# Kernel tuning notes

Measured on AMD Instinct MI355X. Metric: run time of the kernel, lower is better.

The kernel has to match this reference:

```python
import jax, jax.numpy as jnp
import numpy as np

CAP_FACTOR = 1.25


def _moe_top1(x, wg, w1, b1, w2, b2):
    """Top-1 switch MoE with capacity-based token dropping.
    x: [T, d]; wg: [d, E]; w1: [E, d, f]; b1: [E, f]; w2: [E, f, d]; b2: [E, d].
    """
    T, d = x.shape
    E = wg.shape[1]
    cap = int(CAP_FACTOR * T / E)
    probs = jax.nn.softmax(x @ wg, axis=-1)            # [T, E]
    idx = jnp.argmax(probs, axis=-1)                   # [T] expert assignment
    gate = jnp.max(probs, axis=-1)                     # [T] gate prob
    oh = jax.nn.one_hot(idx, E, dtype=jnp.int32)       # [T, E]
    # position of each token within its expert's buffer
    pos = (jnp.cumsum(oh, axis=0) * oh).sum(-1) - 1    # [T]
    keep = pos < cap                                   # drop tokens over capacity
    pos_w = jnp.where(keep, pos, cap)                  # dropped -> overflow slot
    # dispatch: scatter tokens into per-expert buffers [E, cap+1, d]
    buf = jnp.zeros((E, cap + 1, d), dtype=x.dtype).at[idx, pos_w].set(x)
    buf = buf[:, :cap]                                 # slice off overflow slot
    # grouped expert FFN
    h = jax.nn.relu(jnp.einsum('ecd,edf->ecf', buf, w1) + b1[:, None, :])
    eo = jnp.einsum('ecf,efd->ecd', h, w2) + b2[:, None, :]
    # combine: gather each token's expert output, scale by gate prob, zero dropped
    pos_g = jnp.minimum(pos_w, cap - 1)
    out = eo[idx, pos_g] * (gate * keep.astype(x.dtype))[:, None]
    return out


def setup_inputs():
    key = jax.random.key(0)
    ks = jax.random.split(key, 12)
    B, S, d, dff, E1, E2 = 8, 2048, 1024, 4096, 8, 16
    s = lambda fan: np.float32(1.0 / np.sqrt(fan))
    return dict(
        x=jax.random.normal(ks[0], (B, S, d), jnp.float32),
        y=jax.random.randint(ks[1], (B,), 0, d),
        wg1=jax.random.normal(ks[2], (d, E1), jnp.float32) * s(d),
        w1a=jax.random.normal(ks[3], (E1, d, dff), jnp.float32) * s(d),
        b1a=jnp.zeros((E1, dff), jnp.float32),
        w2a=jax.random.normal(ks[4], (E1, dff, d), jnp.float32) * s(dff),
        b2a=jnp.zeros((E1, d), jnp.float32),
        wg2=jax.random.normal(ks[5], (d, E2), jnp.float32) * s(d),
        w1b=jax.random.normal(ks[6], (E2, d, dff), jnp.float32) * s(d),
        b1b=jnp.zeros((E2, dff), jnp.float32),
        w2b=jax.random.normal(ks[7], (E2, dff, d), jnp.float32) * s(dff),
        b2b=jnp.zeros((E2, d), jnp.float32),
    )


def reference(x, y, wg1, w1a, b1a, w2a, b2a, wg2, w1b, b1b, w2b, b2b):
    B, S, d = x.shape
    xf = x.reshape(B * S, d)
    m1 = _moe_top1(xf, wg1, w1a, b1a, w2a, b2a)        # moe1(x)
    m2 = _moe_top1(m1, wg2, w1b, b1b, w2b, b2b)        # moe2(moe_out)
    resid = x + m2.reshape(B, S, d)                    # residual add
    sent = resid.mean(axis=1)                          # [B, d] mean-pool -> logits
    logp = jax.nn.log_softmax(sent, axis=-1)
    return -logp[jnp.arange(B), y].mean()              # cross-entropy loss
```

## Files before the change

kernel.cpp:

```cpp
#include <hip/hip_runtime.h>
#include <hip/hip_bf16.h>
#include <cstdint>
#include <cstddef>

#define B_    8
#define S_    2048
#define D_    1024
#define DFF_  4096
#define E1_   8
#define E2_   16
#define T_    (B_*S_)
#define CAP1_ 2560
#define CAP2_ 1280
#define EC_   20480

typedef __bf16 bf16x8 __attribute__((ext_vector_type(8)));
typedef float  f32x4  __attribute__((ext_vector_type(4)));

__device__ __forceinline__ unsigned short f2bf(float x) {
  return __builtin_bit_cast(unsigned short, (__bf16)x);
}

template<int E>
__global__ __launch_bounds__(256)
void gate_kernel(const float* __restrict__ X, const float* __restrict__ WG,
                 int* __restrict__ idxO, float* __restrict__ gateO) {
  const int lane = threadIdx.x & 63;
  const int wv   = threadIdx.x >> 6;
  const int t    = blockIdx.x * 4 + wv;
  const float* xr = X + (size_t)t * D_;
  float acc[E];
#pragma unroll
  for (int e = 0; e < E; ++e) acc[e] = 0.f;
#pragma unroll
  for (int i = 0; i < 4; ++i) {
    float4 xv = *(const float4*)(xr + i * 256 + lane * 4);
    int kb = i * 256 + lane * 4;
#pragma unroll
    for (int j = 0; j < 4; ++j) {
      float xs = (&xv.x)[j];
      const float* wr = WG + (size_t)(kb + j) * E;
#pragma unroll
      for (int e = 0; e < E; ++e) acc[e] += xs * wr[e];
    }
  }
#pragma unroll
  for (int e = 0; e < E; ++e) {
    float v = acc[e];
#pragma unroll
    for (int s = 32; s >= 1; s >>= 1) v += __shfl_xor(v, s, 64);
    acc[e] = v;
  }
  if (lane == 0) {
    float mx = acc[0]; int mi = 0;
#pragma unroll
    for (int e = 1; e < E; ++e) if (acc[e] > mx) { mx = acc[e]; mi = e; }
    float s = 0.f;
#pragma unroll
    for (int e = 0; e < E; ++e) s += expf(acc[e] - mx);
    idxO[t]  = mi;
    gateO[t] = 1.0f / s;
  }
}

__global__ __launch_bounds__(1024)
void scan_kernel(const int* __restrict__ idx, int E, int cap,
                 int* __restrict__ pos, int* __restrict__ kept) {
  __shared__ int cnt[16][17];
  __shared__ int gbase[16];
  const int tid = threadIdx.x;
  const int w = tid >> 6, lane = tid & 63;
  if (tid < E) gbase[tid] = 0;
  __syncthreads();
  const unsigned long long lt = (lane == 63) ? 0xFFFFFFFFFFFFFFFFull >> 1
                                             : ((1ull << lane) - 1ull);
  for (int it = 0; it < T_ / 1024; ++it) {
    int t = it * 1024 + tid;
    int mi = idx[t];
    int rank = 0;
    for (int e = 0; e < E; ++e) {
      unsigned long long m = __ballot(mi == e);
      if (lane == 0) cnt[w][e] = __popcll(m);
      if (mi == e) rank = __popcll(m & lt);
    }
    __syncthreads();
    int off = 0;
    for (int w2 = 0; w2 < w; ++w2) off += cnt[w2][mi];
    pos[t] = gbase[mi] + off + rank;
    __syncthreads();
    if (tid < E) {
      int tot = 0;
      for (int w2 = 0; w2 < 16; ++w2) tot += cnt[w2][tid];
      gbase[tid] += tot;
    }
    __syncthreads();
  }
  if (tid < E) kept[tid] = min(gbase[tid], cap);
}

__global__ __launch_bounds__(64)
void scatter_kernel(const float* __restrict__ X, const int* __restrict__ idx,
                    const int* __restrict__ pos, int cap,
                    unsigned short* __restrict__ xbuf, int* __restrict__ tokmap,
                    float* __restrict__ mzero) {
  const int t = blockIdx.x;
  const int lane = threadIdx.x;
  const int p = pos[t];
  if (p < cap) {
    const size_t dst = ((size_t)idx[t] * cap + p) * D_;
    const float* xr = X + (size_t)t * D_;
#pragma unroll
    for (int i = 0; i < 4; ++i) {
      float4 v = *(const float4*)(xr + i * 256 + lane * 4);
      ushort4 o;
      o.x = f2bf(v.x); o.y = f2bf(v.y); o.z = f2bf(v.z); o.w = f2bf(v.w);
      *(ushort4*)(xbuf + dst + i * 256 + lane * 4) = o;
    }
    if (lane == 0) tokmap[(size_t)idx[t] * cap + p] = t;
  } else {
    float4 z = {0.f, 0.f, 0.f, 0.f};
    float* mr = mzero + (size_t)t * D_;
#pragma unroll
    for (int i = 0; i < 4; ++i) *(float4*)(mr + i * 256 + lane * 4) = z;
  }
}

__global__ __launch_bounds__(256)
void wtrans_kernel(const float* __restrict__ src, unsigned short* __restrict__ dst,
                   int K, int N) {
  __shared__ float t[64][65];
  const int tid = threadIdx.x;
  const size_t eo = (size_t)blockIdx.z * K * N;
  const int k0 = blockIdx.y * 64, n0 = blockIdx.x * 64;
  const float* s = src + eo + (size_t)k0 * N + n0;
  unsigned short* d = dst + eo + (size_t)n0 * K + k0;
#pragma unroll
  for (int i = 0; i < 4; ++i) {
    int k = i * 16 + (tid >> 4);
    int n4 = (tid & 15) * 4;
    float4 v = *(const float4*)(s + (size_t)k * N + n4);
    t[k][n4] = v.x; t[k][n4 + 1] = v.y; t[k][n4 + 2] = v.z; t[k][n4 + 3] = v.w;
  }
  __syncthreads();
#pragma unroll
  for (int i = 0; i < 4; ++i) {
    int n = i * 16 + (tid >> 4);
    int k4 = (tid & 15) * 4;
    ushort4 o;
    o.x = f2bf(t[k4][n]);     o.y = f2bf(t[k4 + 1][n]);
    o.z = f2bf(t[k4 + 2][n]); o.w = f2bf(t[k4 + 3][n]);
    *(ushort4*)(d + (size_t)n * K + k4) = o;
  }
}

#define STG(BASEPTR, H, KT, SLOT) do {                                          \
    const unsigned short* _s = (BASEPTR) + (size_t)((H) * 128) * K + (KT) + st_off; \
    __builtin_amdgcn_global_load_lds((const __attribute__((address_space(1))) void*)_s, \
        (__attribute__((address_space(3))) void*)(smem + (SLOT) + dst0), 16, 0, 0);   \
    __builtin_amdgcn_global_load_lds((const __attribute__((address_space(1))) void*)(_s + (size_t)64 * K), \
        (__attribute__((address_space(3))) void*)(smem + (SLOT) + 8192 + dst0), 16, 0, 0); \
  } while (0)

#define RDA(BUF, MH) do { _Pragma("unroll")                                     \
    for (int m_ = 0; m_ < 4; ++m_) {                                            \
      const char* _p = smem + (BUF) * 65536 + aslot + ((MH) * 4 + m_) * 2048;   \
      af[m_][0] = *(const bf16x8*)(_p + va);                                    \
      af[m_][1] = *(const bf16x8*)(_p + (va ^ 64)); } } while (0)

#define RDB(BUF, NH) do { _Pragma("unroll")                                     \
    for (int j_ = 0; j_ < 2; ++j_) {                                            \
      const char* _p = smem + (BUF) * 65536 + bslot + ((NH) * 2 + j_) * 2048;   \
      bf[(NH) * 2 + j_][0] = *(const bf16x8*)(_p + vb);                         \
      bf[(NH) * 2 + j_][1] = *(const bf16x8*)(_p + (vb ^ 64)); } } while (0)

#define QUAD(MH, NH) do {                                                       \
    __builtin_amdgcn_s_setprio(1);                                              \
    _Pragma("unroll") for (int m_ = 0; m_ < 4; ++m_)                            \
    _Pragma("unroll") for (int j_ = 0; j_ < 2; ++j_)                            \
    _Pragma("unroll") for (int k_ = 0; k_ < 2; ++k_)                            \
      acc[(MH) * 4 + m_][(NH) * 2 + j_] = __builtin_amdgcn_mfma_f32_16x16x32_bf16( \
          af[m_][k_], bf[(NH) * 2 + j_][k_], acc[(MH) * 4 + m_][(NH) * 2 + j_], 0, 0, 0); \
    __builtin_amdgcn_s_setprio(0);                                              \
  } while (0)

#define SB0   __builtin_amdgcn_sched_barrier(0)
#define BAR   __builtin_amdgcn_s_barrier()
#define VM6   do { asm volatile("s_waitcnt vmcnt(6)" ::: "memory"); SB0; } while (0)
#define VM8   do { asm volatile("s_waitcnt vmcnt(8)" ::: "memory"); SB0; } while (0)
#define VM0   do { asm volatile("s_waitcnt vmcnt(0)" ::: "memory"); SB0; } while (0)

template<int MODE>
__global__ __launch_bounds__(512, 2)
void moe_gemm(const unsigned short* __restrict__ A,
              const unsigned short* __restrict__ BT,
              const float* __restrict__ bias, int K, int N, int cap, int nbcnt,
              const int* __restrict__ kept,
              unsigned short* __restrict__ Hout, float* __restrict__ Mout,
              const int* __restrict__ tokmap, const float* __restrict__ gate) {
  __shared__ char smem[131072];
  const int tid  = threadIdx.x;
  const int lane = tid & 63;
  const int wv   = tid >> 6;
  const int wr   = wv >> 2;
  const int wc   = wv & 3;

  const int nwg = gridDim.x;
  const int wg  = (blockIdx.x & 7) * (nwg >> 3) + (blockIdx.x >> 3);
  const int per_grp = nbcnt * 4;
  const int grp = wg / per_grp;
  const int rem = wg - grp * per_grp;
  const int mb  = grp * 4 + (rem & 3);
  const int nb  = rem >> 2;

  const int e  = (mb * 256) / cap;
  const int r0 = mb * 256 - e * cap;
  const int kept_e = kept[e];
  if (r0 >= kept_e) return;
  const unsigned short* Ab = A + (size_t)(mb * 256) * K;
  const unsigned short* Bb = BT + ((size_t)e * N + (size_t)nb * 256) * K;

  f32x4 acc[8][4];
#pragma unroll
  for (int m = 0; m < 8; ++m)
#pragma unroll
    for (int n = 0; n < 4; ++n) acc[m][n] = (f32x4){0.f, 0.f, 0.f, 0.f};

  const int scol   = ((tid & 7) ^ ((tid >> 3) & 7)) * 8;
  const size_t st_off = (size_t)(tid >> 3) * K + scol;
  const int dst0   = tid * 16;

  const int r16 = lane & 15;
  const int g16 = (lane >> 4) * 16;
  const int swz = (r16 & 7) * 16;
  const int va  = r16 * 128 + (g16 ^ swz);
  const int vb  = (wc & 1) * 8192 + va;
  const int aslot = wr * 16384;
  const int bslot = 32768 + (wc >> 1) * 16384;
  bf16x8 af[4][2], bf[4][2];


  STG(Ab, 0, 0, 0);
  STG(Bb, 0, 0, 32768);
  STG(Bb, 1, 0, 49152);
  STG(Ab, 1, 0, 16384);
  STG(Ab, 0, 64, 65536);
  STG(Bb, 0, 64, 98304);
  STG(Bb, 1, 64, 114688);
  STG(Ab, 1, 64, 81920);
  VM8; BAR;

  const int NT = K >> 6;
  const int NI = K >> 7;
  for (int i = 0; i < NI; ++i) {
    const bool last = (i == NI - 1);
    const bool s2 = (2 * i + 2) < NT;
    const bool s3 = (2 * i + 3) < NT;
    const int kt1 = (2 * i + 1) << 6;
    const int kt2 = (2 * i + 2) << 6;
    const int kt3 = (2 * i + 3) << 6;

    RDA(0, 0); RDB(0, 0);
    if (i > 0) STG(Ab, 1, kt1, 81920);
    BAR; QUAD(0, 0); BAR;
    RDB(0, 1);
    if (s2) STG(Ab, 0, kt2, 0);
    BAR; QUAD(0, 1); BAR;
    RDA(0, 1);
    if (s2) STG(Bb, 0, kt2, 32768);
    BAR; QUAD(1, 1); BAR;
    if (s2) STG(Bb, 1, kt2, 49152);
    if (last) { VM0; } else { VM6; }
    BAR;
    QUAD(1, 0); BAR;
    RDA(1, 0); RDB(1, 0);
    if (s2) STG(Ab, 1, kt2, 16384);
    BAR; QUAD(0, 0); BAR;
    RDB(1, 1);
    if (s3) STG(Ab, 0, kt3, 65536);
    BAR; QUAD(0, 1); BAR;
    RDA(1, 1);
    if (s3) STG(Bb, 0, kt3, 98304);
    BAR; QUAD(1, 1); BAR;
    if (s3) STG(Bb, 1, kt3, 114688);
    if (!last) VM6;
    BAR;
    QUAD(1, 0); BAR;
  }

  const int rg = lane >> 4;
  float bv[4];
#pragma unroll
  for (int n = 0; n < 4; ++n)
    bv[n] = bias[(size_t)e * N + nb * 256 + wc * 64 + n * 16 + r16];

#pragma unroll
  for (int m = 0; m < 8; ++m) {
#pragma unroll
    for (int r = 0; r < 4; ++r) {
      const int lrow = wr * 128 + m * 16 + rg * 4 + r;
      if (MODE == 0) {
        unsigned short* orow = Hout + (size_t)(mb * 256 + lrow) * N + nb * 256;
#pragma unroll
        for (int n = 0; n < 4; ++n) {
          float v = acc[m][n][r] + bv[n];
          orow[wc * 64 + n * 16 + r16] = f2bf(fmaxf(v, 0.f));
        }
      } else {
        const int lr = r0 + lrow;
        if (lr < kept_e) {
          const int tok = tokmap[mb * 256 + lrow];
          const float gsc = gate[tok];
          float* orow = Mout + (size_t)tok * N + nb * 256;
#pragma unroll
          for (int n = 0; n < 4; ++n)
            orow[wc * 64 + n * 16 + r16] = (acc[m][n][r] + bv[n]) * gsc;
        }
      }
    }
  }
}

__global__ __launch_bounds__(256)
void reduce_kernel(const float* __restrict__ X, const float* __restrict__ M2,
                   float* __restrict__ sent) {
  const int c = blockIdx.x * 256 + threadIdx.x;
  const int b = blockIdx.z;
  const int s0 = blockIdx.y * 128;
  float a = 0.f;
  size_t base = ((size_t)b * S_ + s0) * D_ + c;
  for (int s = 0; s < 128; ++s) a += X[base + (size_t)s * D_] + M2[base + (size_t)s * D_];
  atomicAdd(&sent[b * D_ + c], a * (1.0f / (float)S_));
}

__global__ __launch_bounds__(64)
void loss_kernel(const float* __restrict__ sent, const int* __restrict__ y,
                 float* __restrict__ out) {
  const int lane = threadIdx.x;
  float total = 0.f;
  for (int b = 0; b < B_; ++b) {
    const float* s = sent + b * D_;
    float v[16];
    float mx = -1e30f;
#pragma unroll
    for (int i = 0; i < 16; ++i) { v[i] = s[lane + i * 64]; mx = fmaxf(mx, v[i]); }
#pragma unroll
    for (int sh = 32; sh >= 1; sh >>= 1) mx = fmaxf(mx, __shfl_xor(mx, sh, 64));
    float sm = 0.f;
#pragma unroll
    for (int i = 0; i < 16; ++i) sm += expf(v[i] - mx);
#pragma unroll
    for (int sh = 32; sh >= 1; sh >>= 1) sm += __shfl_xor(sm, sh, 64);
    total += logf(sm) + mx - s[y[b]];
  }
  if (lane == 0) out[0] = total * (1.0f / (float)B_);
}

extern "C" void kernel_launch(void* const* d_in, const int* in_sizes, int n_in,
                              void* d_out, int out_size, void* d_ws, size_t ws_size,
                              hipStream_t stream) {
  const float* x   = (const float*)d_in[0];
  const int*   y   = (const int*)d_in[1];
  const float* wg1 = (const float*)d_in[2];
  const float* w1a = (const float*)d_in[3];
  const float* b1a = (const float*)d_in[4];
  const float* w2a = (const float*)d_in[5];
  const float* b2a = (const float*)d_in[6];
  const float* wg2 = (const float*)d_in[7];
  const float* w1b = (const float*)d_in[8];
  const float* b1b = (const float*)d_in[9];
  const float* w2b = (const float*)d_in[10];
  const float* b2b = (const float*)d_in[11];
  float* out = (float*)d_out;
  (void)in_sizes; (void)n_in; (void)out_size; (void)ws_size;

  char* base = (char*)d_ws;
  size_t o = 0;
  auto alloc = [&](size_t bytes) { size_t r = o; o = (o + bytes + 255) & ~(size_t)255; return r; };
  int*   idx1    = (int*)  (base + alloc((size_t)T_ * 4));
  int*   pos1    = (int*)  (base + alloc((size_t)T_ * 4));
  float* gate1   = (float*)(base + alloc((size_t)T_ * 4));
  int*   idx2    = (int*)  (base + alloc((size_t)T_ * 4));
  int*   pos2    = (int*)  (base + alloc((size_t)T_ * 4));
  float* gate2   = (float*)(base + alloc((size_t)T_ * 4));
  int*   kept1   = (int*)  (base + alloc(64 * 4));
  int*   kept2   = (int*)  (base + alloc(64 * 4));
  int*   tokmap1 = (int*)  (base + alloc((size_t)EC_ * 4));
  int*   tokmap2 = (int*)  (base + alloc((size_t)EC_ * 4));
  float* sent    = (float*)(base + alloc((size_t)B_ * D_ * 4));
  float* m1      = (float*)(base + alloc((size_t)T_ * D_ * 4));
  unsigned short* xbuf = (unsigned short*)(base + alloc((size_t)EC_ * D_ * 2));
  unsigned short* h    = (unsigned short*)(base + alloc((size_t)EC_ * DFF_ * 2));
  unsigned short* wT   = (unsigned short*)(base + alloc((size_t)E2_ * D_ * DFF_ * 2));

  hipMemsetAsync(sent, 0, (size_t)B_ * D_ * 4, stream);

  gate_kernel<E1_><<<T_ / 4, 256, 0, stream>>>(x, wg1, idx1, gate1);
  scan_kernel<<<1, 1024, 0, stream>>>(idx1, E1_, CAP1_, pos1, kept1);
  scatter_kernel<<<T_, 64, 0, stream>>>(x, idx1, pos1, CAP1_, xbuf, tokmap1, m1);
  wtrans_kernel<<<dim3(DFF_ / 64, D_ / 64, E1_), 256, 0, stream>>>(w1a, wT, D_, DFF_);
  moe_gemm<0><<<(DFF_ / 256) * (EC_ / 256), 512, 0, stream>>>(
      xbuf, wT, b1a, D_, DFF_, CAP1_, DFF_ / 256, kept1, h, nullptr, nullptr, nullptr);
  wtrans_kernel<<<dim3(D_ / 64, DFF_ / 64, E1_), 256, 0, stream>>>(w2a, wT, DFF_, D_);
  moe_gemm<1><<<(D_ / 256) * (EC_ / 256), 512, 0, stream>>>(
      h, wT, b2a, DFF_, D_, CAP1_, D_ / 256, kept1, nullptr, m1, tokmap1, gate1);

  gate_kernel<E2_><<<T_ / 4, 256, 0, stream>>>(m1, wg2, idx2, gate2);
  scan_kernel<<<1, 1024, 0, stream>>>(idx2, E2_, CAP2_, pos2, kept2);
  scatter_kernel<<<T_, 64, 0, stream>>>(m1, idx2, pos2, CAP2_, xbuf, tokmap2, m1);
  wtrans_kernel<<<dim3(DFF_ / 64, D_ / 64, E2_), 256, 0, stream>>>(w1b, wT, D_, DFF_);
  moe_gemm<0><<<(DFF_ / 256) * (EC_ / 256), 512, 0, stream>>>(
      xbuf, wT, b1b, D_, DFF_, CAP2_, DFF_ / 256, kept2, h, nullptr, nullptr, nullptr);
  wtrans_kernel<<<dim3(D_ / 64, DFF_ / 64, E2_), 256, 0, stream>>>(w2b, wT, DFF_, D_);
  moe_gemm<1><<<(D_ / 256) * (EC_ / 256), 512, 0, stream>>>(
      h, wT, b2b, DFF_, D_, CAP2_, D_ / 256, kept2, nullptr, m1, tokmap2, gate2);

  reduce_kernel<<<dim3(D_ / 256, S_ / 128, B_), 256, 0, stream>>>(x, m1, sent);
  loss_kernel<<<1, 64, 0, stream>>>(sent, y, out);
}
```

Before: 1.297 ms.

## Make MoE GEMM persistent and prefetch next tile during current tile's tail

Converts moe_gemm into a persistent kernel with 256 workgroups that loop over output tiles, skipping tiles beyond each expert's kept count. In the last K iterations of a tile, the first K-slices of the next tile are loaded into shared memory, so the prologue of one tile overlaps the tail of the previous one. This is meant to remove per-workgroup launch and pipeline fill/drain cost and the tail imbalance. The price is more complex control flow, extra registers, and a fixed grid of 256 that relies on 2 workgroups per CU across 128 CUs.

```diff
diff --git a/kernel.cpp b/kernel.cpp
--- a/kernel.cpp
+++ b/kernel.cpp
@@ -194,6 +194,7 @@
 void moe_gemm(const unsigned short* __restrict__ A,
               const unsigned short* __restrict__ BT,
               const float* __restrict__ bias, int K, int N, int cap, int nbcnt,
+              int ntiles,
               const int* __restrict__ kept,
               unsigned short* __restrict__ Hout, float* __restrict__ Mout,
               const int* __restrict__ tokmap, const float* __restrict__ gate) {
@@ -203,27 +204,9 @@
   const int wv   = tid >> 6;
   const int wr   = wv >> 2;
   const int wc   = wv & 3;
-
-  const int nwg = gridDim.x;
-  const int wg  = (blockIdx.x & 7) * (nwg >> 3) + (blockIdx.x >> 3);
+  const int G    = gridDim.x;
   const int per_grp = nbcnt * 4;
-  const int grp = wg / per_grp;
-  const int rem = wg - grp * per_grp;
-  const int mb  = grp * 4 + (rem & 3);
-  const int nb  = rem >> 2;
-
-  const int e  = (mb * 256) / cap;
-  const int r0 = mb * 256 - e * cap;
-  const int kept_e = kept[e];
-  if (r0 >= kept_e) return;
-  const unsigned short* Ab = A + (size_t)(mb * 256) * K;
-  const unsigned short* Bb = BT + ((size_t)e * N + (size_t)nb * 256) * K;
-
-  f32x4 acc[8][4];
-#pragma unroll
-  for (int m = 0; m < 8; ++m)
-#pragma unroll
-    for (int n = 0; n < 4; ++n) acc[m][n] = (f32x4){0.f, 0.f, 0.f, 0.f};
+  const int chunk   = ntiles >> 3;
 
   const int scol   = ((tid & 7) ^ ((tid >> 3) & 7)) * 8;
   const size_t st_off = (size_t)(tid >> 3) * K + scol;
@@ -238,84 +221,139 @@
   const int bslot = 32768 + (wc >> 1) * 16384;
   bf16x8 af[4][2], bf[4][2];
 
-
-  STG(Ab, 0, 0, 0);
-  STG(Bb, 0, 0, 32768);
-  STG(Bb, 1, 0, 49152);
-  STG(Ab, 1, 0, 16384);
-  STG(Ab, 0, 64, 65536);
-  STG(Bb, 0, 64, 98304);
-  STG(Bb, 1, 64, 114688);
-  STG(Ab, 1, 64, 81920);
+  f32x4 acc[8][4];
+#pragma unroll
+  for (int m = 0; m < 8; ++m)
+#pragma unroll
+    for (int n = 0; n < 4; ++n) acc[m][n] = (f32x4){0.f, 0.f, 0.f, 0.f};
+
+  auto tinfo = [&](int t, int& mb, int& nb, int& e, int& r0) {
+    const int wgx = (t & 7) * chunk + (t >> 3);
+    const int grp = wgx / per_grp;
+    const int rem = wgx - grp * per_grp;
+    mb = grp * 4 + (rem & 3);
+    nb = rem >> 2;
+    e  = (mb * 256) / cap;
+    r0 = mb * 256 - e * cap;
+  };
+
+  int tc = blockIdx.x, mbC = 0, nbC = 0, eC = 0, r0C = 0, keptC = 0;
+  for (; tc < ntiles; tc += G) {
+    tinfo(tc, mbC, nbC, eC, r0C);
+    keptC = kept[eC];
+    if (r0C < keptC) break;
+  }
+  if (tc >= ntiles) return;
+  const unsigned short* AbC = A + (size_t)(mbC * 256) * K;
+  const unsigned short* BbC = BT + ((size_t)eC * N + (size_t)nbC * 256) * K;
+
+  int tn = tc + G, mbN = 0, nbN = 0, eN = 0, r0N = 0, keptN = 0;
+  for (; tn < ntiles; tn += G) {
+    tinfo(tn, mbN, nbN, eN, r0N);
+    keptN = kept[eN];
+    if (r0N < keptN) break;
+  }
+  bool hasN = tn < ntiles;
+  const unsigned short* AbN = hasN ? A + (size_t)(mbN * 256) * K : AbC;
+  const unsigned short* BbN = hasN ? BT + ((size_t)eN * N + (size_t)nbN * 256) * K : BbC;
+
+  STG(AbC, 0, 0, 0);
+  STG(BbC, 0, 0, 32768);
+  STG(BbC, 1, 0, 49152);
+  STG(AbC, 1, 0, 16384);
+  STG(AbC, 0, 64, 65536);
+  STG(BbC, 0, 64, 98304);
+  STG(BbC, 1, 64, 114688);
+  STG(AbC, 1, 64, 81920);
   VM8; BAR;
 
-  const int NT = K >> 6;
   const int NI = K >> 7;
-  for (int i = 0; i < NI; ++i) {
-    const bool last = (i == NI - 1);
-    const bool s2 = (2 * i + 2) < NT;
-    const bool s3 = (2 * i + 3) < NT;
-    const int kt1 = (2 * i + 1) << 6;
-    const int kt2 = (2 * i + 2) << 6;
-    const int kt3 = (2 * i + 3) << 6;
-
-    RDA(0, 0); RDB(0, 0);
-    if (i > 0) STG(Ab, 1, kt1, 81920);
-    BAR; QUAD(0, 0); BAR;
-    RDB(0, 1);
-    if (s2) STG(Ab, 0, kt2, 0);
-    BAR; QUAD(0, 1); BAR;
-    RDA(0, 1);
-    if (s2) STG(Bb, 0, kt2, 32768);
-    BAR; QUAD(1, 1); BAR;
-    if (s2) STG(Bb, 1, kt2, 49152);
-    if (last) { VM0; } else { VM6; }
-    BAR;
-    QUAD(1, 0); BAR;
-    RDA(1, 0); RDB(1, 0);
-    if (s2) STG(Ab, 1, kt2, 16384);
-    BAR; QUAD(0, 0); BAR;
-    RDB(1, 1);
-    if (s3) STG(Ab, 0, kt3, 65536);
-    BAR; QUAD(0, 1); BAR;
-    RDA(1, 1);
-    if (s3) STG(Bb, 0, kt3, 98304);
-    BAR; QUAD(1, 1); BAR;
-    if (s3) STG(Bb, 1, kt3, 114688);
-    if (!last) VM6;
-    BAR;
-    QUAD(1, 0); BAR;
-  }
-
-  const int rg = lane >> 4;
-  float bv[4];
-#pragma unroll
-  for (int n = 0; n < 4; ++n)
-    bv[n] = bias[(size_t)e * N + nb * 256 + wc * 64 + n * 16 + r16];
-
-#pragma unroll
-  for (int m = 0; m < 8; ++m) {
-#pragma unroll
-    for (int r = 0; r < 4; ++r) {
-      const int lrow = wr * 128 + m * 16 + rg * 4 + r;
-      if (MODE == 0) {
-        unsigned short* orow = Hout + (size_t)(mb * 256 + lrow) * N + nb * 256;
-#pragma unroll
-        for (int n = 0; n < 4; ++n) {
-          float v = acc[m][n][r] + bv[n];
-          orow[wc * 64 + n * 16 + r16] = f2bf(fmaxf(v, 0.f));
-        }
-      } else {
-        const int lr = r0 + lrow;
-        if (lr < kept_e) {
-          const int tok = tokmap[mb * 256 + lrow];
-          const float gsc = gate[tok];
-          float* orow = Mout + (size_t)tok * N + nb * 256;
-#pragma unroll
-          for (int n = 0; n < 4; ++n)
-            orow[wc * 64 + n * 16 + r16] = (acc[m][n][r] + bv[n]) * gsc;
+  bool first = true;
+
+  for (;;) {
+    for (int i = 0; i < NI; ++i) {
+      const int kt1 = (2 * i + 1) << 6;
+      const int kt2 = (2 * i + 2) << 6;
+      const int kt3 = kt2 + 64;
+      const bool bnd = (kt2 >= K);
+
+      RDA(0, 0); RDB(0, 0);
+      if (i > 0 || !first) STG(AbC, 1, kt1, 81920);
+      BAR; QUAD(0, 0); BAR;
+      RDB(0, 1);
+      if (!bnd) STG(AbC, 0, kt2, 0); else if (hasN) STG(AbN, 0, 0, 0);
+      BAR; QUAD(0, 1); BAR;
+      RDA(0, 1);
+      if (!bnd) STG(BbC, 0, kt2, 32768); else if (hasN) STG(BbN, 0, 0, 32768);
+      BAR; QUAD(1, 1); BAR;
+      if (!bnd) STG(BbC, 1, kt2, 49152); else if (hasN) STG(BbN, 1, 0, 49152);
+      if (bnd && !hasN) { VM0; } else { VM6; }
+      BAR; QUAD(1, 0); BAR;
+      RDA(1, 0); RDB(1, 0);
+      if (!bnd) STG(AbC, 1, kt2, 16384); else if (hasN) STG(AbN, 1, 0, 16384);
+      BAR; QUAD(0, 0); BAR;
+      RDB(1, 1);
+      if (!bnd) STG(AbC, 0, kt3, 65536); else if (hasN) STG(AbN, 0, 64, 65536);
+      BAR; QUAD(0, 1); BAR;
+      RDA(1, 1);
+      if (!bnd) STG(BbC, 0, kt3, 98304); else if (hasN) STG(BbN, 0, 64, 98304);
+      BAR; QUAD(1, 1); BAR;
+      if (!bnd) STG(BbC, 1, kt3, 114688); else if (hasN) STG(BbN, 1, 64, 114688);
+      if (!(bnd && !hasN)) VM6;
+      BAR; QUAD(1, 0); BAR;
+    }
+
+    {
+      const int rg = lane >> 4;
+      float bv[4];
+#pragma unroll
+      for (int n = 0; n < 4; ++n)
+        bv[n] = bias[(size_t)eC * N + nbC * 256 + wc * 64 + n * 16 + r16];
+#pragma unroll
+      for (int m = 0; m < 8; ++m) {
+#pragma unroll
+        for (int r = 0; r < 4; ++r) {
+          const int lrow = wr * 128 + m * 16 + rg * 4 + r;
+          if (MODE == 0) {
+            unsigned short* orow = Hout + (size_t)(mbC * 256 + lrow) * N + nbC * 256;
+#pragma unroll
+            for (int n = 0; n < 4; ++n) {
+              float v = acc[m][n][r] + bv[n];
+              orow[wc * 64 + n * 16 + r16] = f2bf(fmaxf(v, 0.f));
+            }
+          } else {
+            const int lr = r0C + lrow;
+            if (lr < keptC) {
+              const int tok = tokmap[mbC * 256 + lrow];
+              const float gsc = gate[tok];
+              float* orow = Mout + (size_t)tok * N + nbC * 256;
+#pragma unroll
+              for (int n = 0; n < 4; ++n)
+                orow[wc * 64 + n * 16 + r16] = (acc[m][n][r] + bv[n]) * gsc;
+            }
+          }
         }
       }
+#pragma unroll
+      for (int m = 0; m < 8; ++m)
+#pragma unroll
+        for (int n = 0; n < 4; ++n) acc[m][n] = (f32x4){0.f, 0.f, 0.f, 0.f};
+    }
+
+    first = false;
+    if (!hasN) break;
+    tc = tn; mbC = mbN; nbC = nbN; eC = eN; r0C = r0N; keptC = keptN;
+    AbC = AbN; BbC = BbN;
+    tn = tc + G;
+    for (; tn < ntiles; tn += G) {
+      tinfo(tn, mbN, nbN, eN, r0N);
+      keptN = kept[eN];
+      if (r0N < keptN) break;
+    }
+    hasN = tn < ntiles;
+    if (hasN) {
+      AbN = A + (size_t)(mbN * 256) * K;
+      BbN = BT + ((size_t)eN * N + (size_t)nbN * 256) * K;
     }
   }
 }
@@ -394,25 +432,28 @@
 
   hipMemsetAsync(sent, 0, (size_t)B_ * D_ * 4, stream);
 
+  const int NT0 = (DFF_ / 256) * (EC_ / 256);
+  const int NT1 = (D_  / 256) * (EC_ / 256);
+
   gate_kernel<E1_><<<T_ / 4, 256, 0, stream>>>(x, wg1, idx1, gate1);
   scan_kernel<<<1, 1024, 0, stream>>>(idx1, E1_, CAP1_, pos1, kept1);
   scatter_kernel<<<T_, 64, 0, stream>>>(x, idx1, pos1, CAP1_, xbuf, tokmap1, m1);
   wtrans_kernel<<<dim3(DFF_ / 64, D_ / 64, E1_), 256, 0, stream>>>(w1a, wT, D_, DFF_);
-  moe_gemm<0><<<(DFF_ / 256) * (EC_ / 256), 512, 0, stream>>>(
-      xbuf, wT, b1a, D_, DFF_, CAP1_, DFF_ / 256, kept1, h, nullptr, nullptr, nullptr);
+  moe_gemm<0><<<256, 512, 0, stream>>>(
+      xbuf, wT, b1a, D_, DFF_, CAP1_, DFF_ / 256, NT0, kept1, h, nullptr, nullptr, nullptr);
   wtrans_kernel<<<dim3(D_ / 64, DFF_ / 64, E1_), 256, 0, stream>>>(w2a, wT, DFF_, D_);
-  moe_gemm<1><<<(D_ / 256) * (EC_ / 256), 512, 0, stream>>>(
-      h, wT, b2a, DFF_, D_, CAP1_, D_ / 256, kept1, nullptr, m1, tokmap1, gate1);
+  moe_gemm<1><<<256, 512, 0, stream>>>(
+      h, wT, b2a, DFF_, D_, CAP1_, D_ / 256, NT1, kept1, nullptr, m1, tokmap1, gate1);
 
   gate_kernel<E2_><<<T_ / 4, 256, 0, stream>>>(m1, wg2, idx2, gate2);
   scan_kernel<<<1, 1024, 0, stream>>>(idx2, E2_, CAP2_, pos2, kept2);
   scatter_kernel<<<T_, 64, 0, stream>>>(m1, idx2, pos2, CAP2_, xbuf, tokmap2, m1);
   wtrans_kernel<<<dim3(DFF_ / 64, D_ / 64, E2_), 256, 0, stream>>>(w1b, wT, D_, DFF_);
-  moe_gemm<0><<<(DFF_ / 256) * (EC_ / 256), 512, 0, stream>>>(
-      xbuf, wT, b1b, D_, DFF_, CAP2_, DFF_ / 256, kept2, h, nullptr, nullptr, nullptr);
+  moe_gemm<0><<<256, 512, 0, stream>>>(
+      xbuf, wT, b1b, D_, DFF_, CAP2_, DFF_ / 256, NT0, kept2, h, nullptr, nullptr, nullptr);
   wtrans_kernel<<<dim3(D_ / 64, DFF_ / 64, E2_), 256, 0, stream>>>(w2b, wT, DFF_, D_);
-  moe_gemm<1><<<(D_ / 256) * (EC_ / 256), 512, 0, stream>>>(
-      h, wT, b2b, DFF_, D_, CAP2_, D_ / 256, kept2, nullptr, m1, tokmap2, gate2);
+  moe_gemm<1><<<256, 512, 0, stream>>>(
+      h, wT, b2b, DFF_, D_, CAP2_, D_ / 256, NT1, kept2, nullptr, m1, tokmap2, gate2);
 
   reduce_kernel<<<dim3(D_ / 256, S_ / 128, B_), 256, 0, stream>>>(x, m1, sent);
   loss_kernel<<<1, 64, 0, stream>>>(sent, y, out);
```

Result: slower. 1.536 ms (+18.5%).
